# Optimization experiments

Hardware: AMD Instinct MI355X
Metric: run time of the kernel (lower is better)

Reference implementation:

```python
import jax, jax.numpy as jnp
import numpy as np

N_NODES = 50000
N_EDGES = 1600000
IN_FEAT = 256
HIDDEN = 128
N_CLASSES = 16


def gcn_conv(x, edge_index, W, b, n_nodes):
    """PyG GCNConv: x' = D^{-1/2} (A+I) D^{-1/2} (x @ W) + b."""
    h = x @ W  # project first (PyG order), messages are in out_dim
    src, dst = edge_index[0], edge_index[1]
    loops = jnp.arange(n_nodes, dtype=src.dtype)
    src = jnp.concatenate([src, loops])
    dst = jnp.concatenate([dst, loops])
    # degree of A+I (count incoming edges incl. self loop)
    deg = jax.ops.segment_sum(jnp.ones_like(dst, dtype=h.dtype), dst, num_segments=n_nodes)
    dis = jax.lax.rsqrt(deg)  # deg >= 1 thanks to self loops
    norm = dis[src] * dis[dst]  # [E+N]
    msgs = h[src] * norm[:, None]  # gather + scale
    out = jax.ops.segment_sum(msgs, dst, num_segments=n_nodes)  # scatter-add
    return out + b


def setup_inputs() -> dict:
    key = jax.random.key(0)
    k_x, k_e, k_w1, k_b1, k_w2, k_b2 = jax.random.split(key, 6)
    x = jax.random.normal(k_x, (N_NODES, IN_FEAT), dtype=jnp.float32)
    edge_index = jax.random.randint(k_e, (2, N_EDGES), 0, N_NODES, dtype=jnp.int64)
    s1 = 1.0 / np.sqrt(IN_FEAT)
    s2 = 1.0 / np.sqrt(HIDDEN)
    W1 = jax.random.uniform(k_w1, (IN_FEAT, HIDDEN), jnp.float32, -s1, s1)
    b1 = jax.random.uniform(k_b1, (HIDDEN,), jnp.float32, -s1, s1)
    W2 = jax.random.uniform(k_w2, (HIDDEN, N_CLASSES), jnp.float32, -s2, s2)
    b2 = jax.random.uniform(k_b2, (N_CLASSES,), jnp.float32, -s2, s2)
    return {"x": x, "edge_index": edge_index, "W1": W1, "b1": b1, "W2": W2, "b2": b2}


def reference(x, edge_index, W1, b1, W2, b2):
    n = x.shape[0]
    h = gcn_conv(x, edge_index, W1, b1, n)
    h = jax.nn.relu(h)
    logits = gcn_conv(h, edge_index, W2, b2, n)
    return logits, jax.nn.softmax(logits, axis=1)
```

## Files before the change

### kernel.cpp

```cpp
#include <hip/hip_runtime.h>
#include <hip/hip_bf16.h>
#include <math.h>

#define N_NODES 50000
#define N_EDGES 1600000
#define IN_FEAT 256
#define HIDDEN 128
#define N_CLASSES 16

#define ECHUNK 8192
#define NCHK 196
#define NBKT 196
#define BCAP 10240

typedef __attribute__((ext_vector_type(8))) short short8;
typedef __attribute__((ext_vector_type(4))) float floatx4;

__device__ __forceinline__ unsigned short f2bf(float f) {
    unsigned u = __float_as_uint(f);
    return (unsigned short)((u + 0x7fffu + ((u >> 16) & 1u)) >> 16);
}

__device__ __forceinline__ unsigned pk2bf(float a, float b) {
    __hip_bfloat162 h = __float22bfloat162_rn(make_float2(a, b));
    union { __hip_bfloat162 h; unsigned u; } cv;
    cv.h = h;
    return cv.u;
}

__global__ __launch_bounds__(256) void scatter_edges2(const int* __restrict__ src,
                                                      const int* __restrict__ dst,
                                                      int* __restrict__ cursor,
                                                      unsigned int* __restrict__ sorted,
                                                      const float* __restrict__ W1,
                                                      unsigned short* __restrict__ w1t) {
    __shared__ int hloc[256];
    int t = threadIdx.x;
    hloc[t] = 0;
    if (blockIdx.x < HIDDEN)
        w1t[blockIdx.x * IN_FEAT + t] = f2bf(W1[t * HIDDEN + blockIdx.x]);
    __syncthreads();
    int base = blockIdx.x * ECHUNK;
    int end = min(base + ECHUNK, N_EDGES);
    for (int i = base + t; i < end; i += 256)
        atomicAdd(&hloc[dst[i] >> 8], 1);
    __syncthreads();
    int cnt = hloc[t];
    int lbase = t * BCAP + atomicAdd(&cursor[t], cnt);
    __syncthreads();
    hloc[t] = lbase;
    __syncthreads();
    for (int i = base + t; i < end; i += 256) {
        int d = dst[i];
        int s = src[i];
        int pos = atomicAdd(&hloc[d >> 8], 1);
        sorted[pos] = ((unsigned)d << 16) | (unsigned)s;
    }
}

__global__ __launch_bounds__(256) void build_csr2(const unsigned int* __restrict__ sorted,
                                                  const int* __restrict__ cursor,
                                                  int* __restrict__ rs,
                                                  int* __restrict__ re,
                                                  float* __restrict__ dis,
                                                  unsigned short* __restrict__ csr_src) {
    __shared__ int cnt[256];
    __shared__ int roff[256];
    int t = threadIdx.x;
    int bkt = blockIdx.x;
    int ebase = bkt * BCAP;
    int eend = ebase + cursor[bkt];
    cnt[t] = 0;
    __syncthreads();
    for (int i = ebase + t; i < eend; i += 256)
        atomicAdd(&cnt[(sorted[i] >> 16) & 255], 1);
    __syncthreads();
    int v = cnt[t];
    roff[t] = v;
    __syncthreads();
    for (int off = 1; off < 256; off <<= 1) {
        int x = (t >= off) ? roff[t - off] : 0;
        __syncthreads();
        roff[t] += x;
        __syncthreads();
    }
    int excl = roff[t] - v;
    int node = bkt * 256 + t;
    if (node < N_NODES) {
        rs[node] = ebase + excl;
        re[node] = ebase + excl + v;
        dis[node] = 1.0f / sqrtf((float)(v + 1));
    }
    __syncthreads();
    cnt[t] = ebase + excl;
    __syncthreads();
    for (int i = ebase + t; i < eend; i += 256) {
        unsigned e = sorted[i];
        int pos = atomicAdd(&cnt[(e >> 16) & 255], 1);
        csr_src[pos] = (unsigned short)(e & 0xffffu);
    }
}

__global__ __launch_bounds__(256) void gemm1_mfma(const float* __restrict__ x,
                                                  const unsigned short* __restrict__ w1t,
                                                  const float* __restrict__ dis,
                                                  unsigned int* __restrict__ g1) {
    int tid = threadIdx.x;
    int w = tid >> 6;
    int lane = tid & 63;
    int quad = lane >> 4;
    int c = lane & 15;
    int row_base = blockIdx.x * 64 + (w >> 1) * 32;
    int col_base = (w & 1) * 64;

    floatx4 acc[2][4] = {};

    const float* xp[2];
#pragma unroll
    for (int rt = 0; rt < 2; ++rt) {
        int r = min(row_base + rt * 16 + c, N_NODES - 1);
        xp[rt] = x + (size_t)r * IN_FEAT + quad * 8;
    }
    const unsigned short* bp[4];
#pragma unroll
    for (int nt = 0; nt < 4; ++nt)
        bp[nt] = w1t + (size_t)(col_base + nt * 16 + c) * IN_FEAT + quad * 8;

    float4 fa[2][2];
    short8 bcur[4];
#pragma unroll
    for (int rt = 0; rt < 2; ++rt) {
        fa[rt][0] = *(const float4*)(xp[rt] + 0);
        fa[rt][1] = *(const float4*)(xp[rt] + 4);
    }
#pragma unroll
    for (int nt = 0; nt < 4; ++nt)
        bcur[nt] = *(const short8*)(bp[nt] + 0);

#pragma unroll
    for (int kk = 0; kk < 8; ++kk) {
        float4 fn[2][2];
        short8 bn[4];
        if (kk < 7) {
            int k0n = (kk + 1) * 32;
#pragma unroll
            for (int rt = 0; rt < 2; ++rt) {
                fn[rt][0] = *(const float4*)(xp[rt] + k0n);
                fn[rt][1] = *(const float4*)(xp[rt] + k0n + 4);
            }
#pragma unroll
            for (int nt = 0; nt < 4; ++nt)
                bn[nt] = *(const short8*)(bp[nt] + k0n);
        }
        short8 a[2];
#pragma unroll
        for (int rt = 0; rt < 2; ++rt) {
            union { short8 s; unsigned u[4]; } au;
            au.u[0] = pk2bf(fa[rt][0].x, fa[rt][0].y);
            au.u[1] = pk2bf(fa[rt][0].z, fa[rt][0].w);
            au.u[2] = pk2bf(fa[rt][1].x, fa[rt][1].y);
            au.u[3] = pk2bf(fa[rt][1].z, fa[rt][1].w);
            a[rt] = au.s;
        }
#pragma unroll
        for (int rt = 0; rt < 2; ++rt)
#pragma unroll
            for (int nt = 0; nt < 4; ++nt)
                acc[rt][nt] = __builtin_amdgcn_mfma_f32_16x16x32_bf16(a[rt], bcur[nt], acc[rt][nt], 0, 0, 0);
        if (kk < 7) {
#pragma unroll
            for (int rt = 0; rt < 2; ++rt) { fa[rt][0] = fn[rt][0]; fa[rt][1] = fn[rt][1]; }
#pragma unroll
            for (int nt = 0; nt < 4; ++nt) bcur[nt] = bn[nt];
        }
    }

    bool evenlane = (lane & 1) == 0;
#pragma unroll
    for (int rt = 0; rt < 2; ++rt) {
#pragma unroll
        for (int reg = 0; reg < 4; ++reg) {
            int row = row_base + rt * 16 + quad * 4 + reg;
            float dv = dis[min(row, N_NODES - 1)];
#pragma unroll
            for (int nt = 0; nt < 4; ++nt) {
                float v = acc[rt][nt][reg] * dv;
                float vo = __shfl_xor(v, 1);
                if (evenlane && row < N_NODES) {
                    unsigned pkd = (unsigned)f2bf(v) | ((unsigned)f2bf(vo) << 16);
                    g1[(size_t)row * 64 + (col_base >> 1) + nt * 8 + (c >> 1)] = pkd;
                }
            }
        }
    }
}

__global__ __launch_bounds__(256) void agg1_gemm2(const unsigned int* __restrict__ g1,
                                                  const int* __restrict__ rs,
                                                  const int* __restrict__ re,
                                                  const unsigned short* __restrict__ csr_src,
                                                  const float* __restrict__ dis,
                                                  const float* __restrict__ b1,
                                                  const float* __restrict__ W2,
                                                  float* __restrict__ g2) {
    __shared__ float w2s[HIDDEN * N_CLASSES];
    __shared__ float rsh[4][HIDDEN];
    int tid = threadIdx.x;
    for (int i = tid; i < HIDDEN * N_CLASSES; i += 256) w2s[i] = W2[i];
    __syncthreads();

    int wave = tid >> 6;
    int lane = tid & 63;
    int node = blockIdx.x * 4 + wave;

    unsigned su = g1[(size_t)node * 64 + lane];
    float a0x = __uint_as_float(su << 16), a0y = __uint_as_float(su & 0xffff0000u);
    float a1x = 0.f, a1y = 0.f, a2x = 0.f, a2y = 0.f, a3x = 0.f, a3y = 0.f;
    float a4x = 0.f, a4y = 0.f, a5x = 0.f, a5y = 0.f, a6x = 0.f, a6y = 0.f, a7x = 0.f, a7y = 0.f;

    int e0 = rs[node], e1 = re[node];
    int e = e0;
    for (; e + 8 <= e1; e += 8) {
        int s0 = csr_src[e + 0], s1 = csr_src[e + 1], s2 = csr_src[e + 2], s3 = csr_src[e + 3];
        int s4 = csr_src[e + 4], s5 = csr_src[e + 5], s6 = csr_src[e + 6], s7 = csr_src[e + 7];
        unsigned u0 = g1[(size_t)s0 * 64 + lane];
        unsigned u1 = g1[(size_t)s1 * 64 + lane];
        unsigned u2 = g1[(size_t)s2 * 64 + lane];
        unsigned u3 = g1[(size_t)s3 * 64 + lane];
        unsigned u4 = g1[(size_t)s4 * 64 + lane];
        unsigned u5 = g1[(size_t)s5 * 64 + lane];
        unsigned u6 = g1[(size_t)s6 * 64 + lane];
        unsigned u7 = g1[(size_t)s7 * 64 + lane];
        a0x += __uint_as_float(u0 << 16); a0y += __uint_as_float(u0 & 0xffff0000u);
        a1x += __uint_as_float(u1 << 16); a1y += __uint_as_float(u1 & 0xffff0000u);
        a2x += __uint_as_float(u2 << 16); a2y += __uint_as_float(u2 & 0xffff0000u);
        a3x += __uint_as_float(u3 << 16); a3y += __uint_as_float(u3 & 0xffff0000u);
        a4x += __uint_as_float(u4 << 16); a4y += __uint_as_float(u4 & 0xffff0000u);
        a5x += __uint_as_float(u5 << 16); a5y += __uint_as_float(u5 & 0xffff0000u);
        a6x += __uint_as_float(u6 << 16); a6y += __uint_as_float(u6 & 0xffff0000u);
        a7x += __uint_as_float(u7 << 16); a7y += __uint_as_float(u7 & 0xffff0000u);
    }
    for (; e < e1; ++e) {
        int s = csr_src[e];
        unsigned u = g1[(size_t)s * 64 + lane];
        a0x += __uint_as_float(u << 16); a0y += __uint_as_float(u & 0xffff0000u);
    }
    float sx = ((a0x + a1x) + (a2x + a3x)) + ((a4x + a5x) + (a6x + a7x));
    float sy = ((a0y + a1y) + (a2y + a3y)) + ((a4y + a5y) + (a6y + a7y));

    float dv = dis[node];
    float2 bb = ((const float2*)b1)[lane];
    float rx = fmaxf(fmaf(dv, sx, bb.x), 0.f);
    float ry = fmaxf(fmaf(dv, sy, bb.y), 0.f);

    *(float2*)&rsh[wave][lane * 2] = make_float2(rx, ry);

    int grp = lane >> 4;
    int c = lane & 15;
    int f0 = grp * 32;
    float p = 0.f;
#pragma unroll
    for (int k = 0; k < 32; ++k)
        p = fmaf(rsh[wave][f0 + k], w2s[(f0 + k) * N_CLASSES + c], p);
    p += __shfl_xor(p, 16);
    p += __shfl_xor(p, 32);
    if (lane < 16) g2[(size_t)node * N_CLASSES + lane] = dv * p;
}

__global__ __launch_bounds__(256) void agg2_softmax(const float* __restrict__ g2,
                                                    const int* __restrict__ rs,
                                                    const int* __restrict__ re,
                                                    const unsigned short* __restrict__ csr_src,
                                                    const float* __restrict__ dis,
                                                    const float* __restrict__ b2,
                                                    float* __restrict__ out) {
    int tid = threadIdx.x;
    int node = blockIdx.x * 16 + (tid >> 4);
    int c = tid & 15;
    float acc0 = g2[(size_t)node * N_CLASSES + c];
    float acc1 = 0.f, acc2 = 0.f, acc3 = 0.f;
    float acc4 = 0.f, acc5 = 0.f, acc6 = 0.f, acc7 = 0.f;
    int e0 = rs[node], e1 = re[node];
    int e = e0;
    for (; e + 8 <= e1; e += 8) {
        int s0 = csr_src[e + 0], s1 = csr_src[e + 1], s2 = csr_src[e + 2], s3 = csr_src[e + 3];
        int s4 = csr_src[e + 4], s5 = csr_src[e + 5], s6 = csr_src[e + 6], s7 = csr_src[e + 7];
        acc0 += g2[(size_t)s0 * N_CLASSES + c];
        acc1 += g2[(size_t)s1 * N_CLASSES + c];
        acc2 += g2[(size_t)s2 * N_CLASSES + c];
        acc3 += g2[(size_t)s3 * N_CLASSES + c];
        acc4 += g2[(size_t)s4 * N_CLASSES + c];
        acc5 += g2[(size_t)s5 * N_CLASSES + c];
        acc6 += g2[(size_t)s6 * N_CLASSES + c];
        acc7 += g2[(size_t)s7 * N_CLASSES + c];
    }
    for (; e < e1; ++e) {
        int s = csr_src[e];
        acc0 += g2[(size_t)s * N_CLASSES + c];
    }
    acc0 = ((acc0 + acc1) + (acc2 + acc3)) + ((acc4 + acc5) + (acc6 + acc7));
    float logit = fmaf(dis[node], acc0, b2[c]);
    out[(size_t)node * N_CLASSES + c] = logit;
    float m = logit;
    for (int off = 8; off; off >>= 1) m = fmaxf(m, __shfl_xor(m, off));
    float ex = expf(logit - m);
    float s = ex;
    for (int off = 8; off; off >>= 1) s += __shfl_xor(s, off);
    out[(size_t)N_NODES * N_CLASSES + (size_t)node * N_CLASSES + c] = ex / s;
}


extern "C" void kernel_launch(void* const* d_in, const int* in_sizes, int n_in,
                              void* d_out, int out_size, void* d_ws, size_t ws_size,
                              hipStream_t stream) {
    const float* x  = (const float*)d_in[0];
    const int*   ei = (const int*)d_in[1];
    const float* W1 = (const float*)d_in[2];
    const float* b1 = (const float*)d_in[3];
    const float* W2 = (const float*)d_in[4];
    const float* b2 = (const float*)d_in[5];
    float* out = (float*)d_out;

    char* ws = (char*)d_ws;
    size_t off = 0;
    auto alloc = [&](size_t bytes) -> char* {
        char* p = ws + off;
        off = (off + bytes + 511) & ~(size_t)511;
        return p;
    };
    int*   cursor   = (int*)alloc(256 * 4);
    float* dis      = (float*)alloc(N_NODES * 4);
    int*   rs       = (int*)alloc(N_NODES * 4);
    int*   re       = (int*)alloc(N_NODES * 4);
    unsigned short* w1t = (unsigned short*)alloc((size_t)HIDDEN * IN_FEAT * 2);
    unsigned short* csr_src = (unsigned short*)alloc((size_t)NBKT * BCAP * 2);
    unsigned int* g1 = (unsigned int*)alloc((size_t)N_NODES * 64 * 4);
    float* g2       = (float*)alloc((size_t)N_NODES * N_CLASSES * 4);
    unsigned int* sorted = (unsigned int*)g1;
    (void)ws_size; (void)in_sizes; (void)n_in; (void)out_size;

    const int* src = ei;
    const int* dst = ei + N_EDGES;

    hipMemsetAsync(cursor, 0, 256 * 4, stream);
    scatter_edges2<<<NCHK, 256, 0, stream>>>(src, dst, cursor, sorted, W1, w1t);
    build_csr2<<<NBKT, 256, 0, stream>>>(sorted, cursor, rs, re, dis, csr_src);

    gemm1_mfma<<<(N_NODES + 63) / 64, 256, 0, stream>>>(x, w1t, dis, g1);
    agg1_gemm2<<<N_NODES / 4, 256, 0, stream>>>(g1, rs, re, csr_src, dis, b1, W2, g2);
    agg2_softmax<<<N_NODES / 16, 256, 0, stream>>>(g2, rs, re, csr_src, dis, b2, out);
}
```

Before: 249.3 us.

## Stage GEMM1 x tiles via LDS async loads and widen aggregation gathers

GEMM1 now stages the fp32 x tile into double-buffered shared memory with global_load_lds and reads MFMA A-fragments from LDS, replacing per-lane strided register prefetch. This is meant to make the global loads coalesced, at the cost of a block barrier on every k step. The layer-1 aggregation splits each wave into two half-waves that gather 8-byte rows of different neighbours at once, then combines them with a cross-lane shuffle. That halves the gather instructions per edge but adds the shuffle reduction and fewer independent accumulators.

Result: faster. 240.7 us (-3.4%).

```diff
diff --git a/kernel.cpp b/kernel.cpp
--- a/kernel.cpp
+++ b/kernel.cpp
@@ -27,6 +27,9 @@
     cv.h = h;
     return cv.u;
 }
+
+__device__ __forceinline__ float bflo(unsigned u) { return __uint_as_float(u << 16); }
+__device__ __forceinline__ float bfhi(unsigned u) { return __uint_as_float(u & 0xffff0000u); }
 
 __global__ __launch_bounds__(256) void scatter_edges2(const int* __restrict__ src,
                                                       const int* __restrict__ dst,
@@ -101,86 +104,89 @@
     }
 }
 
+#define XCH 260
+
 __global__ __launch_bounds__(256) void gemm1_mfma(const float* __restrict__ x,
                                                   const unsigned short* __restrict__ w1t,
                                                   const float* __restrict__ dis,
                                                   unsigned int* __restrict__ g1) {
+    __shared__ float xs[2][8 * XCH];
     int tid = threadIdx.x;
     int w = tid >> 6;
     int lane = tid & 63;
     int quad = lane >> 4;
     int c = lane & 15;
-    int row_base = blockIdx.x * 64 + (w >> 1) * 32;
+    int row_base = blockIdx.x * 64;
+    int wrow = (w >> 1) * 32;
     int col_base = (w & 1) * 64;
 
+    int st_row = min(row_base + 16 * w + (lane >> 3), N_NODES - 1);
+    int st_row2 = min(row_base + 16 * w + 8 + (lane >> 3), N_NODES - 1);
+    const float* gp1 = x + (size_t)st_row * IN_FEAT + (lane & 7) * 4;
+    const float* gp2 = x + (size_t)st_row2 * IN_FEAT + (lane & 7) * 4;
+
     floatx4 acc[2][4] = {};
-
-    const float* xp[2];
-#pragma unroll
-    for (int rt = 0; rt < 2; ++rt) {
-        int r = min(row_base + rt * 16 + c, N_NODES - 1);
-        xp[rt] = x + (size_t)r * IN_FEAT + quad * 8;
-    }
     const unsigned short* bp[4];
 #pragma unroll
     for (int nt = 0; nt < 4; ++nt)
         bp[nt] = w1t + (size_t)(col_base + nt * 16 + c) * IN_FEAT + quad * 8;
 
-    float4 fa[2][2];
-    short8 bcur[4];
+    int dwoff[2];
 #pragma unroll
     for (int rt = 0; rt < 2; ++rt) {
-        fa[rt][0] = *(const float4*)(xp[rt] + 0);
-        fa[rt][1] = *(const float4*)(xp[rt] + 4);
-    }
-#pragma unroll
-    for (int nt = 0; nt < 4; ++nt)
-        bcur[nt] = *(const short8*)(bp[nt] + 0);
-
+        int rit = wrow + rt * 16 + c;
+        dwoff[rt] = (rit >> 3) * XCH + (rit & 7) * 32 + quad * 8;
+    }
+
+#define STAGE(buf, k0)                                                                  \
+    do {                                                                                \
+        __builtin_amdgcn_global_load_lds(                                               \
+            (const __attribute__((address_space(1))) void*)(gp1 + (k0)),                \
+            (__attribute__((address_space(3))) void*)&xs[buf][(2 * w) * XCH], 16, 0, 0);\
+        __builtin_amdgcn_global_load_lds(                                               \
+            (const __attribute__((address_space(1))) void*)(gp2 + (k0)),                \
+            (__attribute__((address_space(3))) void*)&xs[buf][(2 * w + 1) * XCH], 16, 0, 0);\
+    } while (0)
+
+    STAGE(0, 0);
+    __syncthreads();
+
+    int buf = 0;
 #pragma unroll
     for (int kk = 0; kk < 8; ++kk) {
-        float4 fn[2][2];
-        short8 bn[4];
-        if (kk < 7) {
-            int k0n = (kk + 1) * 32;
-#pragma unroll
-            for (int rt = 0; rt < 2; ++rt) {
-                fn[rt][0] = *(const float4*)(xp[rt] + k0n);
-                fn[rt][1] = *(const float4*)(xp[rt] + k0n + 4);
-            }
-#pragma unroll
-            for (int nt = 0; nt < 4; ++nt)
-                bn[nt] = *(const short8*)(bp[nt] + k0n);
-        }
+        if (kk < 7) STAGE(buf ^ 1, (kk + 1) * 32);
+        short8 b[4];
+#pragma unroll
+        for (int nt = 0; nt < 4; ++nt)
+            b[nt] = *(const short8*)(bp[nt] + kk * 32);
         short8 a[2];
 #pragma unroll
         for (int rt = 0; rt < 2; ++rt) {
+            float4 f0 = *(const float4*)&xs[buf][dwoff[rt]];
+            float4 f1 = *(const float4*)&xs[buf][dwoff[rt] + 4];
             union { short8 s; unsigned u[4]; } au;
-            au.u[0] = pk2bf(fa[rt][0].x, fa[rt][0].y);
-            au.u[1] = pk2bf(fa[rt][0].z, fa[rt][0].w);
-            au.u[2] = pk2bf(fa[rt][1].x, fa[rt][1].y);
-            au.u[3] = pk2bf(fa[rt][1].z, fa[rt][1].w);
+            au.u[0] = pk2bf(f0.x, f0.y);
+            au.u[1] = pk2bf(f0.z, f0.w);
+            au.u[2] = pk2bf(f1.x, f1.y);
+            au.u[3] = pk2bf(f1.z, f1.w);
             a[rt] = au.s;
         }
 #pragma unroll
         for (int rt = 0; rt < 2; ++rt)
 #pragma unroll
             for (int nt = 0; nt < 4; ++nt)
-                acc[rt][nt] = __builtin_amdgcn_mfma_f32_16x16x32_bf16(a[rt], bcur[nt], acc[rt][nt], 0, 0, 0);
-        if (kk < 7) {
-#pragma unroll
-            for (int rt = 0; rt < 2; ++rt) { fa[rt][0] = fn[rt][0]; fa[rt][1] = fn[rt][1]; }
-#pragma unroll
-            for (int nt = 0; nt < 4; ++nt) bcur[nt] = bn[nt];
-        }
-    }
+                acc[rt][nt] = __builtin_amdgcn_mfma_f32_16x16x32_bf16(a[rt], b[nt], acc[rt][nt], 0, 0, 0);
+        __syncthreads();
+        buf ^= 1;
+    }
+#undef STAGE
 
     bool evenlane = (lane & 1) == 0;
 #pragma unroll
     for (int rt = 0; rt < 2; ++rt) {
 #pragma unroll
         for (int reg = 0; reg < 4; ++reg) {
-            int row = row_base + rt * 16 + quad * 4 + reg;
+            int row = row_base + wrow + rt * 16 + quad * 4 + reg;
             float dv = dis[min(row, N_NODES - 1)];
 #pragma unroll
             for (int nt = 0; nt < 4; ++nt) {
@@ -211,49 +217,68 @@
 
     int wave = tid >> 6;
     int lane = tid & 63;
+    int hi = lane >> 5;
+    int m = lane & 31;
     int node = blockIdx.x * 4 + wave;
-
-    unsigned su = g1[(size_t)node * 64 + lane];
-    float a0x = __uint_as_float(su << 16), a0y = __uint_as_float(su & 0xffff0000u);
-    float a1x = 0.f, a1y = 0.f, a2x = 0.f, a2y = 0.f, a3x = 0.f, a3y = 0.f;
-    float a4x = 0.f, a4y = 0.f, a5x = 0.f, a5y = 0.f, a6x = 0.f, a6y = 0.f, a7x = 0.f, a7y = 0.f;
+    const uint2* g = (const uint2*)g1;
+
+    float s0 = 0.f, s1 = 0.f, s2 = 0.f, s3 = 0.f;
+    float t0 = 0.f, t1 = 0.f, t2 = 0.f, t3 = 0.f;
+    if (hi == 0) {
+        uint2 su = g[(size_t)node * 32 + m];
+        s0 = bflo(su.x); s1 = bfhi(su.x); s2 = bflo(su.y); s3 = bfhi(su.y);
+    }
 
     int e0 = rs[node], e1 = re[node];
     int e = e0;
-    for (; e + 8 <= e1; e += 8) {
-        int s0 = csr_src[e + 0], s1 = csr_src[e + 1], s2 = csr_src[e + 2], s3 = csr_src[e + 3];
-        int s4 = csr_src[e + 4], s5 = csr_src[e + 5], s6 = csr_src[e + 6], s7 = csr_src[e + 7];
-        unsigned u0 = g1[(size_t)s0 * 64 + lane];
-        unsigned u1 = g1[(size_t)s1 * 64 + lane];
-        unsigned u2 = g1[(size_t)s2 * 64 + lane];
-        unsigned u3 = g1[(size_t)s3 * 64 + lane];
-        unsigned u4 = g1[(size_t)s4 * 64 + lane];
-        unsigned u5 = g1[(size_t)s5 * 64 + lane];
-        unsigned u6 = g1[(size_t)s6 * 64 + lane];
-        unsigned u7 = g1[(size_t)s7 * 64 + lane];
-        a0x += __uint_as_float(u0 << 16); a0y += __uint_as_float(u0 & 0xffff0000u);
-        a1x += __uint_as_float(u1 << 16); a1y += __uint_as_float(u1 & 0xffff0000u);
-        a2x += __uint_as_float(u2 << 16); a2y += __uint_as_float(u2 & 0xffff0000u);
-        a3x += __uint_as_float(u3 << 16); a3y += __uint_as_float(u3 & 0xffff0000u);
-        a4x += __uint_as_float(u4 << 16); a4y += __uint_as_float(u4 & 0xffff0000u);
-        a5x += __uint_as_float(u5 << 16); a5y += __uint_as_float(u5 & 0xffff0000u);
-        a6x += __uint_as_float(u6 << 16); a6y += __uint_as_float(u6 & 0xffff0000u);
-        a7x += __uint_as_float(u7 << 16); a7y += __uint_as_float(u7 & 0xffff0000u);
-    }
-    for (; e < e1; ++e) {
-        int s = csr_src[e];
-        unsigned u = g1[(size_t)s * 64 + lane];
-        a0x += __uint_as_float(u << 16); a0y += __uint_as_float(u & 0xffff0000u);
-    }
-    float sx = ((a0x + a1x) + (a2x + a3x)) + ((a4x + a5x) + (a6x + a7x));
-    float sy = ((a0y + a1y) + (a2y + a3y)) + ((a4y + a5y) + (a6y + a7y));
+    for (; e + 16 <= e1; e += 16) {
+        int i0 = csr_src[e + 0 + hi], i1 = csr_src[e + 2 + hi];
+        int i2 = csr_src[e + 4 + hi], i3 = csr_src[e + 6 + hi];
+        int i4 = csr_src[e + 8 + hi], i5 = csr_src[e + 10 + hi];
+        int i6 = csr_src[e + 12 + hi], i7 = csr_src[e + 14 + hi];
+        uint2 u0 = g[(size_t)i0 * 32 + m];
+        uint2 u1 = g[(size_t)i1 * 32 + m];
+        uint2 u2 = g[(size_t)i2 * 32 + m];
+        uint2 u3 = g[(size_t)i3 * 32 + m];
+        uint2 u4 = g[(size_t)i4 * 32 + m];
+        uint2 u5 = g[(size_t)i5 * 32 + m];
+        uint2 u6 = g[(size_t)i6 * 32 + m];
+        uint2 u7 = g[(size_t)i7 * 32 + m];
+        s0 += bflo(u0.x); s1 += bfhi(u0.x); s2 += bflo(u0.y); s3 += bfhi(u0.y);
+        t0 += bflo(u1.x); t1 += bfhi(u1.x); t2 += bflo(u1.y); t3 += bfhi(u1.y);
+        s0 += bflo(u2.x); s1 += bfhi(u2.x); s2 += bflo(u2.y); s3 += bfhi(u2.y);
+        t0 += bflo(u3.x); t1 += bfhi(u3.x); t2 += bflo(u3.y); t3 += bfhi(u3.y);
+        s0 += bflo(u4.x); s1 += bfhi(u4.x); s2 += bflo(u4.y); s3 += bfhi(u4.y);
+        t0 += bflo(u5.x); t1 += bfhi(u5.x); t2 += bflo(u5.y); t3 += bfhi(u5.y);
+        s0 += bflo(u6.x); s1 += bfhi(u6.x); s2 += bflo(u6.y); s3 += bfhi(u6.y);
+        t0 += bflo(u7.x); t1 += bfhi(u7.x); t2 += bflo(u7.y); t3 += bfhi(u7.y);
+    }
+    for (; e + 2 <= e1; e += 2) {
+        int i0 = csr_src[e + hi];
+        uint2 u = g[(size_t)i0 * 32 + m];
+        s0 += bflo(u.x); s1 += bfhi(u.x); s2 += bflo(u.y); s3 += bfhi(u.y);
+    }
+    if (e < e1 && hi == 0) {
+        int i0 = csr_src[e];
+        uint2 u = g[(size_t)i0 * 32 + m];
+        s0 += bflo(u.x); s1 += bfhi(u.x); s2 += bflo(u.y); s3 += bfhi(u.y);
+    }
+    s0 += t0; s1 += t1; s2 += t2; s3 += t3;
+    s0 += __shfl_xor(s0, 32);
+    s1 += __shfl_xor(s1, 32);
+    s2 += __shfl_xor(s2, 32);
+    s3 += __shfl_xor(s3, 32);
 
     float dv = dis[node];
-    float2 bb = ((const float2*)b1)[lane];
-    float rx = fmaxf(fmaf(dv, sx, bb.x), 0.f);
-    float ry = fmaxf(fmaf(dv, sy, bb.y), 0.f);
-
-    *(float2*)&rsh[wave][lane * 2] = make_float2(rx, ry);
+    if (hi == 0) {
+        float4 bb = *(const float4*)&b1[4 * m];
+        float4 r;
+        r.x = fmaxf(fmaf(dv, s0, bb.x), 0.f);
+        r.y = fmaxf(fmaf(dv, s1, bb.y), 0.f);
+        r.z = fmaxf(fmaf(dv, s2, bb.z), 0.f);
+        r.w = fmaxf(fmaf(dv, s3, bb.w), 0.f);
+        *(float4*)&rsh[wave][4 * m] = r;
+    }
 
     int grp = lane >> 4;
     int c = lane & 15;
```
